# Kernel tuning notes

Measured on AMD Instinct MI355X. Metric: run time of the kernel, lower is better.

## Reference

```python
import jax, jax.numpy as jnp
from jax import lax
import numpy as np

PATCH = 16
FREQ = 8
TWO_PI = 2.0 * np.pi


def setup_inputs() -> dict:
    key = jax.random.key(0)
    ks = jax.random.split(key, 4)
    B, C, H, W = 8, 64, 128, 128
    E, O, HID = 8, 64, 128
    GATE_C = C + 4 * FREQ  # 96
    x = jax.random.normal(ks[0], (B, C, H, W), dtype=jnp.float32)
    We = jax.random.normal(ks[1], (E, O, C, 3, 3), dtype=jnp.float32) * (1.0 / np.sqrt(C * 9))
    be = jnp.zeros((E, O), dtype=jnp.float32)
    W1 = jax.random.normal(ks[2], (HID, GATE_C), dtype=jnp.float32) * (1.0 / np.sqrt(GATE_C))
    b1 = jnp.zeros((HID,), dtype=jnp.float32)
    W2 = jax.random.normal(ks[3], (E, HID), dtype=jnp.float32) * (1.0 / np.sqrt(HID))
    b2 = jnp.zeros((E,), dtype=jnp.float32)
    return {"x": x, "We": We, "be": be, "W1": W1, "b1": b1, "W2": W2, "b2": b2}


def _fourier_grid(nH, nW, dtype):
    # positional Fourier features of patch centers: [4*FREQ, nH, nW]
    u = (jnp.arange(nH, dtype=dtype) + 0.5) / nH
    v = (jnp.arange(nW, dtype=dtype) + 0.5) / nW
    uu, vv = jnp.meshgrid(u, v, indexing="ij")  # [nH,nW]
    freqs = (2.0 ** jnp.arange(FREQ, dtype=dtype))[:, None, None]
    au = TWO_PI * freqs * uu[None]
    av = TWO_PI * freqs * vv[None]
    return jnp.concatenate([jnp.sin(au), jnp.cos(au), jnp.sin(av), jnp.cos(av)], axis=0)


def reference(x, We, be, W1, b1, W2, b2):
    B, C, H, W = x.shape
    E = We.shape[0]
    P = PATCH
    nH, nW = H // P, W // P

    # --- router gate: per-patch pooled channels + fourier positional feats ---
    xp = x.reshape(B, C, nH, P, nW, P).mean(axis=(3, 5))  # [B,C,nH,nW]
    four = _fourier_grid(nH, nW, x.dtype)  # [4F,nH,nW]
    g = jnp.concatenate([xp, jnp.broadcast_to(four, (B,) + four.shape)], axis=1)  # [B,gate_c,nH,nW]
    h = jax.nn.relu(jnp.einsum("hc,bcij->bhij", W1, g) + b1[None, :, None, None])
    logits = jnp.einsum("eh,bhij->beij", W2, h) + b2[None, :, None, None]
    probs = jax.nn.softmax(logits, axis=1)  # [B,E,nH,nW]

    # --- conv experts (3x3, SAME, ReLU; dropout inactive at eval) ---
    def expert(w, b):
        y = lax.conv_general_dilated(x, w, (1, 1), "SAME",
                                     dimension_numbers=("NCHW", "OIHW", "NCHW"))
        return jax.nn.relu(y + b[None, :, None, None])

    y = jax.vmap(expert)(We, be)  # [E,B,O,H,W]

    # --- combine: broadcast patch gates to pixels and weight-sum experts ---
    gates = jnp.repeat(jnp.repeat(probs, P, axis=2), P, axis=3)  # [B,E,H,W]
    out = jnp.einsum("ebchw,behw->bchw", y, gates)
    return out
```

## Files before the change

kernel.cpp:

```cpp
#include <hip/hip_runtime.h>
#include <math.h>

#define BB 8
#define CC 64
#define HH 128
#define WW 128
#define EE 8
#define OO 64
#define HID 128
#define GATEC 96
#define NP 8
#define PP 16

typedef __attribute__((ext_vector_type(8))) short bf16x8;
typedef __attribute__((ext_vector_type(4))) float f32x4;

static __device__ __forceinline__ unsigned short f2bf(float f) {
  unsigned int u = __builtin_bit_cast(unsigned int, f);
  unsigned int r = (u + 0x7FFFu + ((u >> 16) & 1u)) >> 16;
  return (unsigned short)r;
}

static __device__ __forceinline__ void gll16(const void* g, void* l) {
  __builtin_amdgcn_global_load_lds(
      (const __attribute__((address_space(1))) void*)g,
      (__attribute__((address_space(3))) void*)l, 16, 0, 0);
}

__global__ __launch_bounds__(256) void prep_kernel(
    const float* __restrict__ x,
    const float* __restrict__ W1, const float* __restrict__ b1,
    const float* __restrict__ W2, const float* __restrict__ b2,
    const float* __restrict__ We,
    float* __restrict__ probs, unsigned short* __restrict__ wp) {
  __shared__ float ps[256];
  __shared__ float g[GATEC];
  __shared__ float hbuf[HID];
  __shared__ float lg[EE];

  if (blockIdx.x >= 512) {
    int idx = (blockIdx.x - 512) * 256 + threadIdx.x;
    if (idx < EE * 9 * OO * CC) {
      int c  = idx & 63;
      int o  = (idx >> 6) & 63;
      int et = idx >> 12;
      int t  = et % 9;
      int e  = et / 9;
      float v = We[(((size_t)(e * OO + o) * CC) + c) * 9 + t];
      int dst = (et << 12) + (o << 6) + ((((c >> 3) ^ (o & 7)) << 3) | (c & 7));
      wp[dst] = f2bf(v);
    }
    return;
  }

  int blk = blockIdx.x;
  int b  = blk >> 6;
  int pi = (blk >> 3) & 7;
  int pj = blk & 7;
  int t  = threadIdx.x;

  {
    int c = t >> 2, q = t & 3;
    const float* xb = x + ((size_t)(b * CC + c) * HH + pi * PP + q * 4) * WW + pj * PP;
    float s = 0.f;
    for (int r = 0; r < 4; ++r)
      for (int col = 0; col < PP; ++col)
        s += xb[r * WW + col];
    ps[t] = s;
  }
  __syncthreads();
  if (t < CC) {
    g[t] = (ps[4*t] + ps[4*t+1] + ps[4*t+2] + ps[4*t+3]) * (1.f / 256.f);
  } else if (t < CC + 32) {
    int k = t - CC;
    int fi = k & 7, kind = k >> 3;
    float freq  = (float)(1 << fi);
    float coord = (kind < 2) ? ((pi + 0.5f) / 8.f) : ((pj + 0.5f) / 8.f);
    float a = 6.28318530717958647692f * freq * coord;
    g[t] = (kind & 1) ? cosf(a) : sinf(a);
  }
  __syncthreads();
  if (t < HID) {
    float acc = b1[t];
    const float* w = W1 + (size_t)t * GATEC;
    for (int c = 0; c < GATEC; ++c) acc += w[c] * g[c];
    hbuf[t] = fmaxf(acc, 0.f);
  }
  __syncthreads();
  if (t < EE) {
    float acc = b2[t];
    const float* w = W2 + (size_t)t * HID;
    for (int k = 0; k < HID; ++k) acc += w[k] * hbuf[k];
    lg[t] = acc;
  }
  __syncthreads();
  if (t < EE) {
    float m = lg[0];
    for (int e = 1; e < EE; ++e) m = fmaxf(m, lg[e]);
    float sum = 0.f;
    for (int e = 0; e < EE; ++e) sum += expf(lg[e] - m);
    probs[((size_t)(b * EE + t) * NP + pi) * NP + pj] = expf(lg[t] - m) / sum;
  }
}

__global__ __launch_bounds__(256, 2) void conv_moe(
    const float* __restrict__ x,
    const unsigned short* __restrict__ wp,
    const float* __restrict__ be,
    const float* __restrict__ probs, float* __restrict__ out) {
  int bx0 = blockIdx.x;
  int b   = blockIdx.y;
  int rg = bx0 >> 2, cg = bx0 & 3;
  const int h0 = rg * 8, w0 = cg * 32;
  const int pi = rg >> 1;
  const int pj0 = cg * 2;

  int lane = threadIdx.x & 63;
  int wave = threadIdx.x >> 6;
  int px   = lane & 15;
  int kg   = lane >> 4;

  __shared__ char xs[340 * 128];
  __shared__ char wb[2][16384];

  {
    const char* src = (const char*)wp + (size_t)(wave * 4) * 1024 + lane * 16;
    char* dst = &wb[0][(wave * 4) * 1024];
#pragma unroll
    for (int i = 0; i < 4; ++i)
      gll16(src + i * 1024, dst + i * 1024);
  }

  for (int idx = threadIdx.x; idx < 340 * 8; idx += 256) {
    int j  = idx / 340;
    int sp = idx % 340;
    int r = sp / 34, col = sp % 34;
    int gr = h0 + r - 1, gc = w0 + col - 1;
    bf16x8 v;
    if (gr >= 0 && gr < HH && gc >= 0 && gc < WW) {
      const float* xb = x + ((size_t)(b * CC + j * 8) * HH + gr) * WW + gc;
#pragma unroll
      for (int q = 0; q < 8; ++q) v[q] = (short)f2bf(xb[(size_t)q * HH * WW]);
    } else {
#pragma unroll
      for (int q = 0; q < 8; ++q) v[q] = 0;
    }
    int g = (gr + gc) & 7;
    *(bf16x8*)(xs + sp * 128 + ((j ^ g) & 7) * 16) = v;
  }
  __syncthreads();

  f32x4 outacc[4][4], acc[4][4];
#pragma unroll
  for (int ot = 0; ot < 4; ++ot)
#pragma unroll
    for (int f = 0; f < 4; ++f) { outacc[ot][f] = (f32x4)(0.f); acc[ot][f] = (f32x4)(0.f); }

  const int gl = h0 + w0 - 2 + wave * 2 + px;

#define LOADAW(dst, wt, ks)                                                     \
  {                                                                             \
    _Pragma("unroll")                                                           \
    for (int ot = 0; ot < 4; ++ot)                                              \
      dst[ot] = *(const bf16x8*)((wt) + (ot * 16 + px) * 128 +                  \
                                 (((((ks) << 2) | kg) ^ (px & 7)) << 4));       \
  }

#define LOADBX(dst, dy, dx, ks)                                                 \
  {                                                                             \
    _Pragma("unroll")                                                           \
    for (int f = 0; f < 4; ++f) {                                               \
      int rowp = f >> 1, ch = f & 1;                                            \
      int sp = (wave * 2 + rowp + (dy)) * 34 + ch * 16 + px + (dx);             \
      int slot = (((((ks) << 2) | kg) ^ (gl + rowp + (dy) + (dx))) & 7);        \
      dst[f] = *(const bf16x8*)(xs + sp * 128 + (slot << 4));                   \
    }                                                                           \
  }

#define MFMA16(A, B)                                                            \
  {                                                                             \
    __builtin_amdgcn_s_setprio(1);                                              \
    _Pragma("unroll")                                                           \
    for (int ot = 0; ot < 4; ++ot)                                              \
      _Pragma("unroll")                                                         \
      for (int f = 0; f < 4; ++f)                                               \
        acc[ot][f] = __builtin_amdgcn_mfma_f32_16x16x32_bf16(A[ot], B[f],       \
                                                             acc[ot][f], 0, 0, 0); \
    __builtin_amdgcn_s_setprio(0);                                              \
  }

#define EPILOGUE(eidx)                                                          \
  {                                                                             \
    float gA = probs[((size_t)(b * EE + (eidx)) * NP + pi) * NP + pj0];         \
    float gB = probs[((size_t)(b * EE + (eidx)) * NP + pi) * NP + pj0 + 1];     \
    _Pragma("unroll")                                                           \
    for (int ot = 0; ot < 4; ++ot) {                                            \
      f32x4 bias = *(const f32x4*)(be + (eidx) * OO + ot * 16 + kg * 4);        \
      _Pragma("unroll")                                                         \
      for (int f = 0; f < 4; ++f) {                                             \
        float gt = (f & 1) ? gB : gA;                                           \
        _Pragma("unroll")                                                       \
        for (int r = 0; r < 4; ++r) {                                           \
          outacc[ot][f][r] += gt * fmaxf(acc[ot][f][r] + bias[r], 0.f);         \
          acc[ot][f][r] = 0.f;                                                  \
        }                                                                       \
      }                                                                         \
    }                                                                           \
  }

  bf16x8 A0[4], B0[4], A1[4], B1[4];
  int e = 0, t9A = 0, dyA = 0, dxA = 0;

  for (int u = 0; u < 36; ++u) {
    int cur = u & 1;
    if (u < 35) {
      const char* src = (const char*)wp + (size_t)(u + 1) * 16384 + (wave * 4) * 1024 + lane * 16;
      char* dst = &wb[cur ^ 1][(wave * 4) * 1024];
#pragma unroll
      for (int i = 0; i < 4; ++i)
        gll16(src + i * 1024, dst + i * 1024);
    }
    int t9B = t9A + 1, dyB = dyA, dxB = dxA + 1;
    if (dxB == 3) { dxB = 0; dyB += 1; }
    if (t9B == 9) { t9B = 0; dyB = 0; dxB = 0; }
    const char* wtA = &wb[cur][0];
    const char* wtB = &wb[cur][8192];

    LOADAW(A0, wtA, 0); LOADBX(B0, dyA, dxA, 0);
    LOADAW(A1, wtA, 1); LOADBX(B1, dyA, dxA, 1);
    MFMA16(A0, B0);
    LOADAW(A0, wtB, 0); LOADBX(B0, dyB, dxB, 0);
    MFMA16(A1, B1);
    if (t9A == 8) { EPILOGUE(e); ++e; }
    LOADAW(A1, wtB, 1); LOADBX(B1, dyB, dxB, 1);
    MFMA16(A0, B0);
    MFMA16(A1, B1);
    if (t9B == 8) { EPILOGUE(e); ++e; }

    t9A = t9B + 1; dyA = dyB; dxA = dxB + 1;
    if (dxA == 3) { dxA = 0; dyA += 1; }
    if (t9A == 9) { t9A = 0; dyA = 0; dxA = 0; }
    __syncthreads();
  }

#pragma unroll
  for (int ot = 0; ot < 4; ++ot) {
#pragma unroll
    for (int f = 0; f < 4; ++f) {
      int rowp = f >> 1, ch = f & 1;
      int o = ot * 16 + kg * 4;
      int h = h0 + wave * 2 + rowp;
      float* op = out + ((size_t)(b * OO + o) * HH + h) * WW + w0 + ch * 16 + px;
#pragma unroll
      for (int r = 0; r < 4; ++r)
        op[(size_t)r * HH * WW] = outacc[ot][f][r];
    }
  }
#undef LOADAW
#undef LOADBX
#undef MFMA16
#undef EPILOGUE
}

extern "C" void kernel_launch(void* const* d_in, const int* in_sizes, int n_in,
                              void* d_out, int out_size, void* d_ws, size_t ws_size,
                              hipStream_t stream) {
  const float* x  = (const float*)d_in[0];
  const float* We = (const float*)d_in[1];
  const float* be = (const float*)d_in[2];
  const float* W1 = (const float*)d_in[3];
  const float* b1 = (const float*)d_in[4];
  const float* W2 = (const float*)d_in[5];
  const float* b2 = (const float*)d_in[6];
  float* out = (float*)d_out;

  float* probs = (float*)d_ws;
  unsigned short* wpk = (unsigned short*)((char*)d_ws + 16384);

  prep_kernel<<<dim3(512 + (EE * 9 * OO * CC + 255) / 256), dim3(256), 0, stream>>>(
      x, W1, b1, W2, b2, We, probs, wpk);
  conv_moe<<<dim3(16 * 4, BB), dim3(256), 0, stream>>>(x, wpk, be, probs, out);
}
```

Before: 103.1 us.

## Load expert weights directly from global into registers, dropping LDS staging

```diff
diff --git a/kernel.cpp b/kernel.cpp
--- a/kernel.cpp
+++ b/kernel.cpp
@@ -21,12 +21,6 @@
   return (unsigned short)r;
 }
 
-static __device__ __forceinline__ void gll16(const void* g, void* l) {
-  __builtin_amdgcn_global_load_lds(
-      (const __attribute__((address_space(1))) void*)g,
-      (__attribute__((address_space(3))) void*)l, 16, 0, 0);
-}
-
 __global__ __launch_bounds__(256) void prep_kernel(
     const float* __restrict__ x,
     const float* __restrict__ W1, const float* __restrict__ b1,
@@ -47,7 +41,8 @@
       int t  = et % 9;
       int e  = et / 9;
       float v = We[(((size_t)(e * OO + o) * CC) + c) * 9 + t];
-      int dst = (et << 12) + (o << 6) + ((((c >> 3) ^ (o & 7)) << 3) | (c & 7));
+      int dst = (et << 12) + (((c >> 5) * 4 + (o >> 4)) << 9)
+              + ((((c >> 3) & 3) * 16 + (o & 15)) << 3) + (c & 7);
       wp[dst] = f2bf(v);
     }
     return;
@@ -121,15 +116,6 @@
   int kg   = lane >> 4;
 
   __shared__ char xs[340 * 128];
-  __shared__ char wb[2][16384];
-
-  {
-    const char* src = (const char*)wp + (size_t)(wave * 4) * 1024 + lane * 16;
-    char* dst = &wb[0][(wave * 4) * 1024];
-#pragma unroll
-    for (int i = 0; i < 4; ++i)
-      gll16(src + i * 1024, dst + i * 1024);
-  }
 
   for (int idx = threadIdx.x; idx < 340 * 8; idx += 256) {
     int j  = idx / 340;
@@ -158,12 +144,14 @@
 
   const int gl = h0 + w0 - 2 + wave * 2 + px;
 
-#define LOADAW(dst, wt, ks)                                                     \
-  {                                                                             \
-    _Pragma("unroll")                                                           \
-    for (int ot = 0; ot < 4; ++ot)                                              \
-      dst[ot] = *(const bf16x8*)((wt) + (ot * 16 + px) * 128 +                  \
-                                 (((((ks) << 2) | kg) ^ (px & 7)) << 4));       \
+  const unsigned short* wq = wp + lane * 8;
+
+#define LOADW(bank, tap)                                                        \
+  {                                                                             \
+    const unsigned short* wt_ = wq + (size_t)(tap) * 4096;                      \
+    _Pragma("unroll")                                                           \
+    for (int i = 0; i < 8; ++i)                                                 \
+      bank[i] = *(const bf16x8*)(wt_ + i * 512);                                \
   }
 
 #define LOADBX(dst, dy, dx, ks)                                                 \
@@ -177,14 +165,23 @@
     }                                                                           \
   }
 
-#define MFMA16(A, B)                                                            \
-  {                                                                             \
+#define TAP(bank, dy, dx)                                                       \
+  {                                                                             \
+    bf16x8 bx0[4], bx1[4];                                                      \
+    LOADBX(bx0, dy, dx, 0);                                                     \
+    LOADBX(bx1, dy, dx, 1);                                                     \
     __builtin_amdgcn_s_setprio(1);                                              \
     _Pragma("unroll")                                                           \
     for (int ot = 0; ot < 4; ++ot)                                              \
       _Pragma("unroll")                                                         \
       for (int f = 0; f < 4; ++f)                                               \
-        acc[ot][f] = __builtin_amdgcn_mfma_f32_16x16x32_bf16(A[ot], B[f],       \
+        acc[ot][f] = __builtin_amdgcn_mfma_f32_16x16x32_bf16(bank[ot], bx0[f],  \
+                                                             acc[ot][f], 0, 0, 0); \
+    _Pragma("unroll")                                                           \
+    for (int ot = 0; ot < 4; ++ot)                                              \
+      _Pragma("unroll")                                                         \
+      for (int f = 0; f < 4; ++f)                                               \
+        acc[ot][f] = __builtin_amdgcn_mfma_f32_16x16x32_bf16(bank[4 + ot], bx1[f], \
                                                              acc[ot][f], 0, 0, 0); \
     __builtin_amdgcn_s_setprio(0);                                              \
   }
@@ -208,39 +205,24 @@
     }                                                                           \
   }
 
-  bf16x8 A0[4], B0[4], A1[4], B1[4];
-  int e = 0, t9A = 0, dyA = 0, dxA = 0;
-
+#define ADVANCE()                                                               \
+  {                                                                             \
+    if (t9 == 8) { EPILOGUE(e); ++e; t9 = 0; dy = 0; dx = 0; }                  \
+    else { ++t9; if (++dx == 3) { dx = 0; ++dy; } }                             \
+  }
+
+  bf16x8 awA[8], awB[8];
+  LOADW(awA, 0);
+  LOADW(awB, 1);
+
+  int e = 0, t9 = 0, dy = 0, dx = 0;
   for (int u = 0; u < 36; ++u) {
-    int cur = u & 1;
-    if (u < 35) {
-      const char* src = (const char*)wp + (size_t)(u + 1) * 16384 + (wave * 4) * 1024 + lane * 16;
-      char* dst = &wb[cur ^ 1][(wave * 4) * 1024];
-#pragma unroll
-      for (int i = 0; i < 4; ++i)
-        gll16(src + i * 1024, dst + i * 1024);
-    }
-    int t9B = t9A + 1, dyB = dyA, dxB = dxA + 1;
-    if (dxB == 3) { dxB = 0; dyB += 1; }
-    if (t9B == 9) { t9B = 0; dyB = 0; dxB = 0; }
-    const char* wtA = &wb[cur][0];
-    const char* wtB = &wb[cur][8192];
-
-    LOADAW(A0, wtA, 0); LOADBX(B0, dyA, dxA, 0);
-    LOADAW(A1, wtA, 1); LOADBX(B1, dyA, dxA, 1);
-    MFMA16(A0, B0);
-    LOADAW(A0, wtB, 0); LOADBX(B0, dyB, dxB, 0);
-    MFMA16(A1, B1);
-    if (t9A == 8) { EPILOGUE(e); ++e; }
-    LOADAW(A1, wtB, 1); LOADBX(B1, dyB, dxB, 1);
-    MFMA16(A0, B0);
-    MFMA16(A1, B1);
-    if (t9B == 8) { EPILOGUE(e); ++e; }
-
-    t9A = t9B + 1; dyA = dyB; dxA = dxB + 1;
-    if (dxA == 3) { dxA = 0; dyA += 1; }
-    if (t9A == 9) { t9A = 0; dyA = 0; dxA = 0; }
-    __syncthreads();
+    TAP(awA, dy, dx);
+    if (u < 35) LOADW(awA, 2 * u + 2);
+    ADVANCE();
+    TAP(awB, dy, dx);
+    if (u < 35) LOADW(awB, 2 * u + 3);
+    ADVANCE();
   }
 
 #pragma unroll
@@ -256,10 +238,11 @@
         op[(size_t)r * HH * WW] = outacc[ot][f][r];
     }
   }
-#undef LOADAW
+#undef LOADW
 #undef LOADBX
-#undef MFMA16
+#undef TAP
 #undef EPILOGUE
+#undef ADVANCE
 }
 
 extern "C" void kernel_launch(void* const* d_in, const int* in_sizes, int n_in,
```

Result: faster. 99.25 us (-3.7%).
